# Kernel optimization log

Measured on AMD Instinct MI355X. Metric: run time of the kernel, lower is better.

Reference implementation:

```python
import jax, jax.numpy as jnp
import numpy as np

B, SQ, SK, D, H = 4, 2048, 2048, 1024, 16
HD = D // H


def setup_inputs() -> dict:
    key = jax.random.key(0)
    ks = jax.random.split(key, 8)
    s = 1.0 / np.sqrt(D)
    return {
        "query": jax.random.normal(ks[0], (B, SQ, D), jnp.float32),
        "key_value": jax.random.normal(ks[1], (B, SK, D), jnp.float32),
        "Wq": jax.random.normal(ks[2], (D, D), jnp.float32) * s,
        "bq": jnp.zeros((D,), jnp.float32),
        "Wkv": jax.random.normal(ks[3], (D, 2 * D), jnp.float32) * s,
        "bkv": jnp.zeros((2 * D,), jnp.float32),
        "Wo": jax.random.normal(ks[4], (D, D), jnp.float32) * s,
        "bo": jnp.zeros((D,), jnp.float32),
    }


def reference(query, key_value, Wq, bq, Wkv, bkv, Wo, bo):
    b, sq, _ = query.shape
    sk = key_value.shape[1]
    # Q projection -> [b, H, sq, HD]
    Q = (query @ Wq + bq).reshape(b, sq, H, HD).transpose(0, 2, 1, 3)
    # fused KV projection -> [b, sk, 2, H, HD]
    KV = (key_value @ Wkv + bkv).reshape(b, sk, 2, H, HD)
    K = KV[:, :, 0].transpose(0, 2, 1, 3)  # [b, H, sk, HD]
    V = KV[:, :, 1].transpose(0, 2, 1, 3)
    scale = 1.0 / np.sqrt(HD).astype(np.float32)
    scores = jnp.einsum("bhqd,bhkd->bhqk", Q, K) * scale
    attn = jax.nn.softmax(scores, axis=-1)  # dropout is identity in eval / p=0
    out = jnp.einsum("bhqk,bhkd->bhqd", attn, V)
    out = out.transpose(0, 2, 1, 3).reshape(b, sq, D)
    return out @ Wo + bo
```

## Files before the change

kernel.cpp:

```cpp
#include <hip/hip_runtime.h>
#include <hip/hip_bf16.h>
#include <stdint.h>


typedef __bf16 bf16_t;
typedef __bf16 bf16x8 __attribute__((ext_vector_type(8)));
typedef __bf16 bf16x4 __attribute__((ext_vector_type(4)));
typedef short  s16x4  __attribute__((ext_vector_type(4)));
typedef float  f32x4  __attribute__((ext_vector_type(4)));

#define MFMA16x32(a, b, c) __builtin_amdgcn_mfma_f32_16x16x32_bf16((a), (b), (c), 0, 0, 0)

__device__ __forceinline__ f32x4 mfma16x16(bf16x4 a, bf16x4 b, f32x4 c) {
#if __has_builtin(__builtin_amdgcn_mfma_f32_16x16x16_bf16)
    return __builtin_amdgcn_mfma_f32_16x16x16_bf16(a, b, c, 0, 0, 0);
#else
    return __builtin_amdgcn_mfma_f32_16x16x16bf16_1k(
        __builtin_bit_cast(s16x4, a), __builtin_bit_cast(s16x4, b), c, 0, 0, 0);
#endif
}

__device__ __forceinline__ float fast_exp2(float x) {
#if __has_builtin(__builtin_amdgcn_exp2f)
    return __builtin_amdgcn_exp2f(x);
#else
    return exp2f(x);
#endif
}

__device__ __forceinline__ void gload16(const void* g, const void* l) {
    __builtin_amdgcn_global_load_lds(
        (__attribute__((address_space(1))) void*)(uintptr_t)g,
        (__attribute__((address_space(3))) void*)(uintptr_t)l,
        16, 0, 0);
}

#define ATTN_SCALE 0.18033688011112042f

__global__ void cvt_bf16_2(const float* __restrict__ a, const float* __restrict__ b,
                           bf16_t* __restrict__ oa, bf16_t* __restrict__ ob) {
    int bid = blockIdx.x;
    const float* in;
    bf16_t* out;
    if (bid < 4096) { in = a; out = oa; }
    else            { in = b; out = ob; bid -= 4096; }
    int i = (bid * 256 + threadIdx.x) * 8;
    const float4* p = (const float4*)(in + i);
    float4 x = p[0], y = p[1];
    bf16x8 v;
    v[0] = (bf16_t)x.x; v[1] = (bf16_t)x.y; v[2] = (bf16_t)x.z; v[3] = (bf16_t)x.w;
    v[4] = (bf16_t)y.x; v[5] = (bf16_t)y.y; v[6] = (bf16_t)y.z; v[7] = (bf16_t)y.w;
    *(bf16x8*)(out + i) = v;
}

__global__ void transpose_cvt3(const float* __restrict__ Wq, const float* __restrict__ Wkv,
                               const float* __restrict__ Wo, bf16_t* __restrict__ WqT,
                               bf16_t* __restrict__ WkvT, bf16_t* __restrict__ WoT) {
    const float* W;
    bf16_t* WT;
    int N;
    if (blockIdx.z == 0)      { W = Wq;  WT = WqT;  N = 1024; }
    else if (blockIdx.z == 1) { W = Wkv; WT = WkvT; N = 2048; }
    else                      { W = Wo;  WT = WoT;  N = 1024; }
    if ((int)blockIdx.x * 64 >= N) return;
    const int K = 1024;
    __shared__ float tile[64][65];
    const int t = threadIdx.x;
    const int n0 = blockIdx.x * 64, k0 = blockIdx.y * 64;
#pragma unroll
    for (int i = 0; i < 16; ++i) {
        int idx = i * 256 + t;
        int r = idx >> 6, c = idx & 63;
        tile[r][c] = W[(size_t)(k0 + r) * N + n0 + c];
    }
    __syncthreads();
#pragma unroll
    for (int i = 0; i < 16; ++i) {
        int idx = i * 256 + t;
        int r = idx >> 6, c = idx & 63;
        WT[(size_t)(n0 + r) * K + k0 + c] = (bf16_t)tile[c][r];
    }
}

template <int MODE>
__global__ __launch_bounds__(256, 3)
void gemm_bt(const bf16_t* __restrict__ A, const bf16_t* __restrict__ BT,
             const float* __restrict__ bias, void* __restrict__ out0,
             void* __restrict__ out1, int M, int N, int K) {
    constexpr int SMEM = (MODE == 1) ? (16384 + 4 * 64 * 72 * 2) : 16384;
    __shared__ __align__(16) char pool[SMEM];
    bf16_t* sA = (bf16_t*)pool;
    bf16_t* sB = (bf16_t*)(pool + 8192);

    const int tid  = threadIdx.x;
    const int lane = tid & 63, w = tid >> 6;
    const int wr = w >> 1, wc = w & 1;
    const int quad = lane >> 4, l15 = lane & 15;
    const int x3 = l15 & 3;
    const int row0 = blockIdx.y * 128, col0 = blockIdx.x * 128;

    f32x4 acc[4][4];
    const f32x4 fz = {0.f, 0.f, 0.f, 0.f};
#pragma unroll
    for (int m = 0; m < 4; ++m)
#pragma unroll
        for (int n = 0; n < 4; ++n) acc[m][n] = fz;

    for (int kt = 0; kt < K; kt += 32) {
#pragma unroll
        for (int i = 0; i < 2; ++i) {
            int c = i * 256 + tid;
            int r = c >> 2, cr = c & 3;
            int g = cr ^ (r & 3);
            gload16(A + (size_t)(row0 + r) * K + kt + g * 8,
                    (const char*)sA + i * 4096 + w * 1024);
            gload16(BT + (size_t)(col0 + r) * K + kt + g * 8,
                    (const char*)sB + i * 4096 + w * 1024);
        }
        __syncthreads();

        bf16x8 af[4], bfr[4];
#pragma unroll
        for (int m = 0; m < 4; ++m)
            af[m] = *(const bf16x8*)(sA + (wr * 64 + m * 16 + l15) * 32 + (quad ^ x3) * 8);
#pragma unroll
        for (int n = 0; n < 4; ++n)
            bfr[n] = *(const bf16x8*)(sB + (wc * 64 + n * 16 + l15) * 32 + (quad ^ x3) * 8);
#pragma unroll
        for (int m = 0; m < 4; ++m)
#pragma unroll
            for (int n = 0; n < 4; ++n)
                acc[m][n] = MFMA16x32(af[m], bfr[n], acc[m][n]);
        __syncthreads();
    }

    if constexpr (MODE == 1) {
        if (col0 >= 1024) {
            bf16_t* sT = (bf16_t*)(pool + 16384) + w * (64 * 72);
            const int j0  = col0 - 1024 + wc * 64;
            const int hh  = j0 >> 6;
            const int sk0 = row0 + wr * 64;
            const int bb  = sk0 >> 11;
            const int skl = sk0 & 2047;
#pragma unroll
            for (int n = 0; n < 4; ++n) {
                int hd = n * 16 + l15;
                float bv = bias[1024 + j0 + n * 16 + l15];
#pragma unroll
                for (int m = 0; m < 4; ++m) {
                    bf16x4 v4;
                    v4[0] = (bf16_t)(acc[m][n][0] + bv);
                    v4[1] = (bf16_t)(acc[m][n][1] + bv);
                    v4[2] = (bf16_t)(acc[m][n][2] + bv);
                    v4[3] = (bf16_t)(acc[m][n][3] + bv);
                    *(bf16x4*)(sT + hd * 72 + m * 16 + quad * 4) = v4;
                }
            }
            bf16_t* vdst = (bf16_t*)out1 +
                           (((size_t)(bb * 16 + hh) * 64) << 11) + skl;
#pragma unroll
            for (int it = 0; it < 8; ++it) {
                int hd = it * 8 + (lane >> 3);
                int sc = (lane & 7) * 8;
                bf16x8 v = *(const bf16x8*)(sT + hd * 72 + sc);
                *(bf16x8*)(vdst + ((size_t)hd << 11) + sc) = v;
            }
            return;
        }
    }

#pragma unroll
    for (int m = 0; m < 4; ++m) {
        int rg_base = row0 + wr * 64 + m * 16 + quad * 4;
#pragma unroll
        for (int n = 0; n < 4; ++n) {
            int cg = col0 + wc * 64 + n * 16 + l15;
            float bv = bias[cg];
#pragma unroll
            for (int r = 0; r < 4; ++r) {
                int rg = rg_base + r;
                float v = acc[m][n][r] + bv;
                if constexpr (MODE == 2) {
                    ((float*)out0)[(size_t)rg * N + cg] = v;
                } else if constexpr (MODE == 0) {
                    v *= ATTN_SCALE;
                    int bb = rg >> 11, sq = rg & 2047;
                    int hh = cg >> 6, hd = cg & 63;
                    ((bf16_t*)out0)[(((size_t)(bb * 16 + hh) * 2048 + sq) << 6) | hd] =
                        (bf16_t)v;
                } else {
                    int bb = rg >> 11, sk = rg & 2047;
                    int hh = cg >> 6, hd = cg & 63;
                    ((bf16_t*)out0)[(((size_t)(bb * 16 + hh) * 2048 + sk) << 6) | hd] =
                        (bf16_t)v;
                }
            }
        }
    }
}

__global__ __launch_bounds__(256, 3)
void attn_kernel(const bf16_t* __restrict__ Qp, const bf16_t* __restrict__ Kb,
                 const bf16_t* __restrict__ Vt, bf16_t* __restrict__ Ob) {
    __shared__ __align__(16) char pool[40960];
    bf16_t* sQ   = (bf16_t*)pool;
    float*  redO = (float*)pool;
    float*  redL = (float*)(pool + 32768);

    const int tid = threadIdx.x;
    const int lane = tid & 63, w = tid >> 6;
    const int quad = lane >> 4, l15 = lane & 15;
    const int x7 = l15 & 7;
    const int qt = blockIdx.x, h = blockIdx.y, b = blockIdx.z;
    const size_t bh = (size_t)b * 16 + h;

    const bf16_t* Qg = Qp + bh * (2048 * 64) + (size_t)qt * (64 * 64);
    const bf16_t* Kg = Kb + bh * (2048 * 64);
    const bf16_t* Vg = Vt + bh * (64 * 2048);

    const int srow = tid >> 3;
    const int sg   = (tid & 7) ^ (srow & 7);

#pragma unroll
    for (int hh = 0; hh < 2; ++hh) {
        int row = hh * 32 + srow;
        gload16(Qg + (size_t)row * 64 + sg * 8, pool + hh * 4096 + w * 1024);
        gload16(Kg + (size_t)row * 64 + sg * 8, pool + 8192 + hh * 4096 + w * 1024);
        gload16(Vg + (size_t)row * 2048 + sg * 8, pool + 24576 + hh * 4096 + w * 1024);
    }
    __syncthreads();

    bf16x8 qf[4][2];
#pragma unroll
    for (int qb = 0; qb < 4; ++qb)
#pragma unroll
        for (int hh = 0; hh < 2; ++hh)
            qf[qb][hh] = *(const bf16x8*)(sQ + (qb * 16 + l15) * 64 +
                                          ((hh * 4 + quad) ^ x7) * 8);

    const f32x4 fz = {0.f, 0.f, 0.f, 0.f};
    f32x4 o_[4][4];
#pragma unroll
    for (int qb = 0; qb < 4; ++qb)
#pragma unroll
        for (int nh = 0; nh < 4; ++nh) o_[qb][nh] = fz;
    float lsum[4] = {0.f, 0.f, 0.f, 0.f};

    for (int t = 0; t < 32; ++t) {
        if (t < 31) {
            const bf16_t* Kt = Kg + (size_t)(t + 1) * (64 * 64);
            char* kb_ = pool + 8192 + ((t + 1) & 1) * 8192;
            char* vb_ = pool + 24576 + ((t + 1) & 1) * 8192;
#pragma unroll
            for (int hh = 0; hh < 2; ++hh) {
                int row = hh * 32 + srow;
                gload16(Kt + (size_t)row * 64 + sg * 8, kb_ + hh * 4096 + w * 1024);
                gload16(Vg + (size_t)row * 2048 + (t + 1) * 64 + sg * 8,
                        vb_ + hh * 4096 + w * 1024);
            }
        }
        const bf16_t* k0 = (const bf16_t*)(pool + 8192 + (t & 1) * 8192);
        const bf16_t* v0 = (const bf16_t*)(pool + 24576 + (t & 1) * 8192);

        const bf16_t* krow = k0 + (w * 16 + l15) * 64;
        bf16x8 kf0 = *(const bf16x8*)(krow + (quad ^ x7) * 8);
        bf16x8 kf1 = *(const bf16x8*)(krow + ((quad + 4) ^ x7) * 8);

        f32x4 s[4];
#pragma unroll
        for (int qb = 0; qb < 4; ++qb) {
            s[qb] = MFMA16x32(kf0, qf[qb][0], fz);
            s[qb] = MFMA16x32(kf1, qf[qb][1], s[qb]);
        }

        bf16x4 pf[4];
#pragma unroll
        for (int qb = 0; qb < 4; ++qb) {
            float p0 = fast_exp2(s[qb][0]);
            float p1 = fast_exp2(s[qb][1]);
            float p2 = fast_exp2(s[qb][2]);
            float p3 = fast_exp2(s[qb][3]);
            lsum[qb] += (p0 + p1) + (p2 + p3);
            bf16x4 pv = {(bf16_t)p0, (bf16_t)p1, (bf16_t)p2, (bf16_t)p3};
            pf[qb] = pv;
        }

        const int vslot = (2 * w + (quad >> 1)) ^ x7;
        const int vsub  = (quad & 1) * 4;
#pragma unroll
        for (int nh = 0; nh < 4; ++nh) {
            bf16x4 vf = *(const bf16x4*)(v0 + (nh * 16 + l15) * 64 + vslot * 8 + vsub);
#pragma unroll
            for (int qb = 0; qb < 4; ++qb)
                o_[qb][nh] = mfma16x16(pf[qb], vf, o_[qb][nh]);
        }
        __syncthreads();
    }

#pragma unroll
    for (int qb = 0; qb < 4; ++qb) {
        lsum[qb] += __shfl_xor(lsum[qb], 16);
        lsum[qb] += __shfl_xor(lsum[qb], 32);
    }
    if (quad == 0) {
#pragma unroll
        for (int qb = 0; qb < 4; ++qb) redL[w * 64 + qb * 16 + l15] = lsum[qb];
    }

    const int cq = tid >> 2;
    const int chb = (tid & 3) * 8;
    const size_t orow = (size_t)b * 2048 + (size_t)qt * 64 + cq;

#pragma unroll
    for (int ph = 0; ph < 2; ++ph) {
        __syncthreads();
#pragma unroll
        for (int qb = 0; qb < 4; ++qb)
#pragma unroll
            for (int nj = 0; nj < 2; ++nj) {
                int nh = ph * 2 + nj;
#pragma unroll
                for (int r = 0; r < 4; ++r)
                    redO[w * 2048 + (qb * 16 + quad * 4 + r) * 32 + nj * 16 + l15] =
                        o_[qb][nh][r];
            }
        __syncthreads();

        float lt = redL[cq] + redL[64 + cq] + redL[128 + cq] + redL[192 + cq];
        float linv = 1.f / lt;
        float4 a0 = {0, 0, 0, 0}, a1 = {0, 0, 0, 0};
#pragma unroll
        for (int ww = 0; ww < 4; ++ww) {
            const float4* p = (const float4*)(redO + ww * 2048 + cq * 32 + chb);
            float4 x = p[0], y = p[1];
            a0.x += x.x; a0.y += x.y; a0.z += x.z; a0.w += x.w;
            a1.x += y.x; a1.y += y.y; a1.z += y.z; a1.w += y.w;
        }
        bf16x8 ov;
        ov[0] = (bf16_t)(a0.x * linv); ov[1] = (bf16_t)(a0.y * linv);
        ov[2] = (bf16_t)(a0.z * linv); ov[3] = (bf16_t)(a0.w * linv);
        ov[4] = (bf16_t)(a1.x * linv); ov[5] = (bf16_t)(a1.y * linv);
        ov[6] = (bf16_t)(a1.z * linv); ov[7] = (bf16_t)(a1.w * linv);
        *(bf16x8*)(Ob + orow * 1024 + h * 64 + ph * 32 + chb) = ov;
    }
}

extern "C" void kernel_launch(void* const* d_in, const int* in_sizes, int n_in,
                              void* d_out, int out_size, void* d_ws, size_t ws_size,
                              hipStream_t stream) {
    const float* query     = (const float*)d_in[0];
    const float* key_value = (const float*)d_in[1];
    const float* Wq  = (const float*)d_in[2];
    const float* bq  = (const float*)d_in[3];
    const float* Wkv = (const float*)d_in[4];
    const float* bkv = (const float*)d_in[5];
    const float* Wo  = (const float*)d_in[6];
    const float* bo  = (const float*)d_in[7];
    float* out = (float*)d_out;

    char* ws = (char*)d_ws;
    const size_t MB = 1024 * 1024;
    bf16_t* WqT  = (bf16_t*)(ws + 0 * MB);
    bf16_t* WkvT = (bf16_t*)(ws + 2 * MB);
    bf16_t* WoT  = (bf16_t*)(ws + 6 * MB);
    bf16_t* qb   = (bf16_t*)(ws + 8 * MB);
    bf16_t* kvb  = (bf16_t*)(ws + 24 * MB);
    bf16_t* Qp   = (bf16_t*)(ws + 40 * MB);
    bf16_t* Kb   = (bf16_t*)(ws + 56 * MB);
    bf16_t* Vt   = (bf16_t*)(ws + 72 * MB);
    bf16_t* Ob   = (bf16_t*)(ws + 88 * MB);

    cvt_bf16_2<<<8192, 256, 0, stream>>>(query, key_value, qb, kvb);
    transpose_cvt3<<<dim3(32, 16, 3), 256, 0, stream>>>(Wq, Wkv, Wo, WqT, WkvT, WoT);

    gemm_bt<0><<<dim3(8, 64), 256, 0, stream>>>(qb, WqT, bq, Qp, nullptr,
                                                8192, 1024, 1024);
    gemm_bt<1><<<dim3(16, 64), 256, 0, stream>>>(kvb, WkvT, bkv, Kb, Vt,
                                                 8192, 2048, 1024);
    attn_kernel<<<dim3(32, 16, 4), 256, 0, stream>>>(Qp, Kb, Vt, Ob);
    gemm_bt<2><<<dim3(8, 64), 256, 0, stream>>>(Ob, WoT, bo, out, nullptr,
                                                8192, 1024, 1024);
}
```

Before: 333.7 us.

## Merge prep and QKV launches, move softmax row sums to MFMA, trim attention LDS

The two preprocessing kernels become one launch, and the Q and KV projection GEMMs become one grid, so fewer kernels run and the tail of one can overlap the head of the next. In attention, the softmax denominator is now accumulated by an MFMA against a ones vector, replacing VALU adds and cross-lane shuffles. The V double buffer reuses the Q staging area, which lowers LDS use so the launch bound can rise to 4 blocks per CU. Risks: the row sums are now taken from bf16-rounded probabilities, the added MFMA work competes with the PV product, and the larger occupancy target could cause register spills.

```diff
diff --git a/kernel.cpp b/kernel.cpp
--- a/kernel.cpp
+++ b/kernel.cpp
@@ -37,36 +37,40 @@
 
 #define ATTN_SCALE 0.18033688011112042f
 
-__global__ void cvt_bf16_2(const float* __restrict__ a, const float* __restrict__ b,
-                           bf16_t* __restrict__ oa, bf16_t* __restrict__ ob) {
+__global__ void prep_kernel(const float* __restrict__ q, const float* __restrict__ kv,
+                            const float* __restrict__ Wq, const float* __restrict__ Wkv,
+                            const float* __restrict__ Wo, bf16_t* __restrict__ qb,
+                            bf16_t* __restrict__ kvb, bf16_t* __restrict__ WqT,
+                            bf16_t* __restrict__ WkvT, bf16_t* __restrict__ WoT) {
+    __shared__ float tile[64][65];
     int bid = blockIdx.x;
-    const float* in;
-    bf16_t* out;
-    if (bid < 4096) { in = a; out = oa; }
-    else            { in = b; out = ob; bid -= 4096; }
-    int i = (bid * 256 + threadIdx.x) * 8;
-    const float4* p = (const float4*)(in + i);
-    float4 x = p[0], y = p[1];
-    bf16x8 v;
-    v[0] = (bf16_t)x.x; v[1] = (bf16_t)x.y; v[2] = (bf16_t)x.z; v[3] = (bf16_t)x.w;
-    v[4] = (bf16_t)y.x; v[5] = (bf16_t)y.y; v[6] = (bf16_t)y.z; v[7] = (bf16_t)y.w;
-    *(bf16x8*)(out + i) = v;
-}
-
-__global__ void transpose_cvt3(const float* __restrict__ Wq, const float* __restrict__ Wkv,
-                               const float* __restrict__ Wo, bf16_t* __restrict__ WqT,
-                               bf16_t* __restrict__ WkvT, bf16_t* __restrict__ WoT) {
+    const int t = threadIdx.x;
+    if (bid < 8192) {
+        const float* in;
+        bf16_t* out;
+        if (bid < 4096) { in = q; out = qb; }
+        else            { in = kv; out = kvb; bid -= 4096; }
+        int i = (bid * 256 + t) * 8;
+        const float4* p = (const float4*)(in + i);
+        float4 x = p[0], y = p[1];
+        bf16x8 v;
+        v[0] = (bf16_t)x.x; v[1] = (bf16_t)x.y; v[2] = (bf16_t)x.z; v[3] = (bf16_t)x.w;
+        v[4] = (bf16_t)y.x; v[5] = (bf16_t)y.y; v[6] = (bf16_t)y.z; v[7] = (bf16_t)y.w;
+        *(bf16x8*)(out + i) = v;
+        return;
+    }
+    bid -= 8192;
+    int z = bid >> 9, rem = bid & 511;
+    int xb = rem & 31, yb = rem >> 5;
     const float* W;
     bf16_t* WT;
     int N;
-    if (blockIdx.z == 0)      { W = Wq;  WT = WqT;  N = 1024; }
-    else if (blockIdx.z == 1) { W = Wkv; WT = WkvT; N = 2048; }
-    else                      { W = Wo;  WT = WoT;  N = 1024; }
-    if ((int)blockIdx.x * 64 >= N) return;
+    if (z == 0)      { W = Wq;  WT = WqT;  N = 1024; }
+    else if (z == 1) { W = Wkv; WT = WkvT; N = 2048; }
+    else             { W = Wo;  WT = WoT;  N = 1024; }
+    if (xb * 64 >= N) return;
     const int K = 1024;
-    __shared__ float tile[64][65];
-    const int t = threadIdx.x;
-    const int n0 = blockIdx.x * 64, k0 = blockIdx.y * 64;
+    const int n0 = xb * 64, k0 = yb * 64;
 #pragma unroll
     for (int i = 0; i < 16; ++i) {
         int idx = i * 256 + t;
@@ -82,13 +86,13 @@
     }
 }
 
-template <int MODE>
 __global__ __launch_bounds__(256, 3)
-void gemm_bt(const bf16_t* __restrict__ A, const bf16_t* __restrict__ BT,
-             const float* __restrict__ bias, void* __restrict__ out0,
-             void* __restrict__ out1, int M, int N, int K) {
-    constexpr int SMEM = (MODE == 1) ? (16384 + 4 * 64 * 72 * 2) : 16384;
-    __shared__ __align__(16) char pool[SMEM];
+void gemm_qkv(const bf16_t* __restrict__ qb, const bf16_t* __restrict__ kvb,
+              const bf16_t* __restrict__ WqT, const bf16_t* __restrict__ WkvT,
+              const float* __restrict__ bq, const float* __restrict__ bkv,
+              bf16_t* __restrict__ Qp, bf16_t* __restrict__ Kb,
+              bf16_t* __restrict__ Vt) {
+    __shared__ __align__(16) char pool[16384 + 4 * 64 * 72 * 2];
     bf16_t* sA = (bf16_t*)pool;
     bf16_t* sB = (bf16_t*)(pool + 8192);
 
@@ -97,7 +101,13 @@
     const int wr = w >> 1, wc = w & 1;
     const int quad = lane >> 4, l15 = lane & 15;
     const int x3 = l15 & 3;
-    const int row0 = blockIdx.y * 128, col0 = blockIdx.x * 128;
+    const bool isQ = blockIdx.x < 8;
+    const bf16_t* A    = isQ ? qb : kvb;
+    const bf16_t* BT   = isQ ? WqT : WkvT;
+    const float*  bias = isQ ? bq : bkv;
+    const int row0 = blockIdx.y * 128;
+    const int col0 = (isQ ? blockIdx.x : (blockIdx.x - 8)) * 128;
+    const int K = 1024;
 
     f32x4 acc[4][4];
     const f32x4 fz = {0.f, 0.f, 0.f, 0.f};
@@ -134,39 +144,36 @@
         __syncthreads();
     }
 
-    if constexpr (MODE == 1) {
-        if (col0 >= 1024) {
-            bf16_t* sT = (bf16_t*)(pool + 16384) + w * (64 * 72);
-            const int j0  = col0 - 1024 + wc * 64;
-            const int hh  = j0 >> 6;
-            const int sk0 = row0 + wr * 64;
-            const int bb  = sk0 >> 11;
-            const int skl = sk0 & 2047;
-#pragma unroll
-            for (int n = 0; n < 4; ++n) {
-                int hd = n * 16 + l15;
-                float bv = bias[1024 + j0 + n * 16 + l15];
-#pragma unroll
-                for (int m = 0; m < 4; ++m) {
-                    bf16x4 v4;
-                    v4[0] = (bf16_t)(acc[m][n][0] + bv);
-                    v4[1] = (bf16_t)(acc[m][n][1] + bv);
-                    v4[2] = (bf16_t)(acc[m][n][2] + bv);
-                    v4[3] = (bf16_t)(acc[m][n][3] + bv);
-                    *(bf16x4*)(sT + hd * 72 + m * 16 + quad * 4) = v4;
-                }
+    if (!isQ && col0 >= 1024) {
+        bf16_t* sT = (bf16_t*)(pool + 16384) + w * (64 * 72);
+        const int j0  = col0 - 1024 + wc * 64;
+        const int hh  = j0 >> 6;
+        const int sk0 = row0 + wr * 64;
+        const int bb  = sk0 >> 11;
+        const int skl = sk0 & 2047;
+#pragma unroll
+        for (int n = 0; n < 4; ++n) {
+            int hd = n * 16 + l15;
+            float bv = bkv[1024 + j0 + n * 16 + l15];
+#pragma unroll
+            for (int m = 0; m < 4; ++m) {
+                bf16x4 v4;
+                v4[0] = (bf16_t)(acc[m][n][0] + bv);
+                v4[1] = (bf16_t)(acc[m][n][1] + bv);
+                v4[2] = (bf16_t)(acc[m][n][2] + bv);
+                v4[3] = (bf16_t)(acc[m][n][3] + bv);
+                *(bf16x4*)(sT + hd * 72 + m * 16 + quad * 4) = v4;
             }
-            bf16_t* vdst = (bf16_t*)out1 +
-                           (((size_t)(bb * 16 + hh) * 64) << 11) + skl;
-#pragma unroll
-            for (int it = 0; it < 8; ++it) {
-                int hd = it * 8 + (lane >> 3);
-                int sc = (lane & 7) * 8;
-                bf16x8 v = *(const bf16x8*)(sT + hd * 72 + sc);
-                *(bf16x8*)(vdst + ((size_t)hd << 11) + sc) = v;
-            }
-            return;
-        }
+        }
+        bf16_t* vdst = Vt + (((size_t)(bb * 16 + hh) * 64) << 11) + skl;
+#pragma unroll
+        for (int it = 0; it < 8; ++it) {
+            int hd = it * 8 + (lane >> 3);
+            int sc = (lane & 7) * 8;
+            bf16x8 v = *(const bf16x8*)(sT + hd * 72 + sc);
+            *(bf16x8*)(vdst + ((size_t)hd << 11) + sc) = v;
+        }
+        return;
     }
 
 #pragma unroll
@@ -180,29 +187,82 @@
             for (int r = 0; r < 4; ++r) {
                 int rg = rg_base + r;
                 float v = acc[m][n][r] + bv;
-                if constexpr (MODE == 2) {
-                    ((float*)out0)[(size_t)rg * N + cg] = v;
-                } else if constexpr (MODE == 0) {
-                    v *= ATTN_SCALE;
-                    int bb = rg >> 11, sq = rg & 2047;
-                    int hh = cg >> 6, hd = cg & 63;
-                    ((bf16_t*)out0)[(((size_t)(bb * 16 + hh) * 2048 + sq) << 6) | hd] =
-                        (bf16_t)v;
-                } else {
-                    int bb = rg >> 11, sk = rg & 2047;
-                    int hh = cg >> 6, hd = cg & 63;
-                    ((bf16_t*)out0)[(((size_t)(bb * 16 + hh) * 2048 + sk) << 6) | hd] =
-                        (bf16_t)v;
-                }
+                int bb = rg >> 11, sr = rg & 2047;
+                int hh = cg >> 6, hd = cg & 63;
+                size_t idx = (((size_t)(bb * 16 + hh) * 2048 + sr) << 6) | hd;
+                if (isQ) Qp[idx] = (bf16_t)(v * ATTN_SCALE);
+                else     Kb[idx] = (bf16_t)v;
             }
         }
     }
 }
 
 __global__ __launch_bounds__(256, 3)
+void gemm_out(const bf16_t* __restrict__ A, const bf16_t* __restrict__ BT,
+              const float* __restrict__ bias, float* __restrict__ out,
+              int M, int N, int K) {
+    __shared__ __align__(16) bf16_t sA[128 * 32];
+    __shared__ __align__(16) bf16_t sB[128 * 32];
+    const int tid  = threadIdx.x;
+    const int lane = tid & 63, w = tid >> 6;
+    const int wr = w >> 1, wc = w & 1;
+    const int quad = lane >> 4, l15 = lane & 15;
+    const int x3 = l15 & 3;
+    const int row0 = blockIdx.y * 128, col0 = blockIdx.x * 128;
+
+    f32x4 acc[4][4];
+    const f32x4 fz = {0.f, 0.f, 0.f, 0.f};
+#pragma unroll
+    for (int m = 0; m < 4; ++m)
+#pragma unroll
+        for (int n = 0; n < 4; ++n) acc[m][n] = fz;
+
+    for (int kt = 0; kt < K; kt += 32) {
+#pragma unroll
+        for (int i = 0; i < 2; ++i) {
+            int c = i * 256 + tid;
+            int r = c >> 2, cr = c & 3;
+            int g = cr ^ (r & 3);
+            gload16(A + (size_t)(row0 + r) * K + kt + g * 8,
+                    (const char*)sA + i * 4096 + w * 1024);
+            gload16(BT + (size_t)(col0 + r) * K + kt + g * 8,
+                    (const char*)sB + i * 4096 + w * 1024);
+        }
+        __syncthreads();
+
+        bf16x8 af[4], bfr[4];
+#pragma unroll
+        for (int m = 0; m < 4; ++m)
+            af[m] = *(const bf16x8*)(sA + (wr * 64 + m * 16 + l15) * 32 + (quad ^ x3) * 8);
+#pragma unroll
+        for (int n = 0; n < 4; ++n)
+            bfr[n] = *(const bf16x8*)(sB + (wc * 64 + n * 16 + l15) * 32 + (quad ^ x3) * 8);
+#pragma unroll
+        for (int m = 0; m < 4; ++m)
+#pragma unroll
+            for (int n = 0; n < 4; ++n)
+                acc[m][n] = MFMA16x32(af[m], bfr[n], acc[m][n]);
+        __syncthreads();
+    }
+
+#pragma unroll
+    for (int m = 0; m < 4; ++m) {
+        int rg_base = row0 + wr * 64 + m * 16 + quad * 4;
+#pragma unroll
+        for (int n = 0; n < 4; ++n) {
+            int cg = col0 + wc * 64 + n * 16 + l15;
+            float bv = bias[cg];
+#pragma unroll
+            for (int r = 0; r < 4; ++r)
+                out[(size_t)(rg_base + r) * N + cg] = acc[m][n][r] + bv;
+        }
+    }
+}
+
+__global__ __launch_bounds__(256, 4)
 void attn_kernel(const bf16_t* __restrict__ Qp, const bf16_t* __restrict__ Kb,
                  const bf16_t* __restrict__ Vt, bf16_t* __restrict__ Ob) {
-    __shared__ __align__(16) char pool[40960];
+    __shared__ __align__(16) char pool[36864];
     bf16_t* sQ   = (bf16_t*)pool;
     float*  redO = (float*)pool;
     float*  redL = (float*)(pool + 32768);
@@ -237,20 +297,24 @@
         for (int hh = 0; hh < 2; ++hh)
             qf[qb][hh] = *(const bf16x8*)(sQ + (qb * 16 + l15) * 64 +
                                           ((hh * 4 + quad) ^ x7) * 8);
+    __syncthreads();
 
     const f32x4 fz = {0.f, 0.f, 0.f, 0.f};
+    const bf16x4 ones = {(bf16_t)1.f, (bf16_t)1.f, (bf16_t)1.f, (bf16_t)1.f};
     f32x4 o_[4][4];
-#pragma unroll
-    for (int qb = 0; qb < 4; ++qb)
+    f32x4 lacc[4];
+#pragma unroll
+    for (int qb = 0; qb < 4; ++qb) {
+        lacc[qb] = fz;
 #pragma unroll
         for (int nh = 0; nh < 4; ++nh) o_[qb][nh] = fz;
-    float lsum[4] = {0.f, 0.f, 0.f, 0.f};
+    }
 
     for (int t = 0; t < 32; ++t) {
         if (t < 31) {
             const bf16_t* Kt = Kg + (size_t)(t + 1) * (64 * 64);
-            char* kb_ = pool + 8192 + ((t + 1) & 1) * 8192;
-            char* vb_ = pool + 24576 + ((t + 1) & 1) * 8192;
+            char* kb_ = pool + 8192 + (((t + 1) & 1) << 13);
+            char* vb_ = ((t + 1) & 1) ? pool : pool + 24576;
 #pragma unroll
             for (int hh = 0; hh < 2; ++hh) {
                 int row = hh * 32 + srow;
@@ -259,8 +323,8 @@
                         vb_ + hh * 4096 + w * 1024);
             }
         }
-        const bf16_t* k0 = (const bf16_t*)(pool + 8192 + (t & 1) * 8192);
-        const bf16_t* v0 = (const bf16_t*)(pool + 24576 + (t & 1) * 8192);
+        const bf16_t* k0 = (const bf16_t*)(pool + 8192 + ((t & 1) << 13));
+        const bf16_t* v0 = (const bf16_t*)((t & 1) ? pool : pool + 24576);
 
         const bf16_t* krow = k0 + (w * 16 + l15) * 64;
         bf16x8 kf0 = *(const bf16x8*)(krow + (quad ^ x7) * 8);
@@ -276,13 +340,13 @@
         bf16x4 pf[4];
 #pragma unroll
         for (int qb = 0; qb < 4; ++qb) {
-            float p0 = fast_exp2(s[qb][0]);
-            float p1 = fast_exp2(s[qb][1]);
-            float p2 = fast_exp2(s[qb][2]);
-            float p3 = fast_exp2(s[qb][3]);
-            lsum[qb] += (p0 + p1) + (p2 + p3);
-            bf16x4 pv = {(bf16_t)p0, (bf16_t)p1, (bf16_t)p2, (bf16_t)p3};
+            bf16x4 pv;
+            pv[0] = (bf16_t)fast_exp2(s[qb][0]);
+            pv[1] = (bf16_t)fast_exp2(s[qb][1]);
+            pv[2] = (bf16_t)fast_exp2(s[qb][2]);
+            pv[3] = (bf16_t)fast_exp2(s[qb][3]);
             pf[qb] = pv;
+            lacc[qb] = mfma16x16(pf[qb], ones, lacc[qb]);
         }
 
         const int vslot = (2 * w + (quad >> 1)) ^ x7;
@@ -297,14 +361,12 @@
         __syncthreads();
     }
 
-#pragma unroll
-    for (int qb = 0; qb < 4; ++qb) {
-        lsum[qb] += __shfl_xor(lsum[qb], 16);
-        lsum[qb] += __shfl_xor(lsum[qb], 32);
-    }
-    if (quad == 0) {
-#pragma unroll
-        for (int qb = 0; qb < 4; ++qb) redL[w * 64 + qb * 16 + l15] = lsum[qb];
+    if (l15 == 0) {
+#pragma unroll
+        for (int qb = 0; qb < 4; ++qb)
+#pragma unroll
+            for (int r = 0; r < 4; ++r)
+                redL[w * 64 + qb * 16 + quad * 4 + r] = lacc[qb][r];
     }
 
     const int cq = tid >> 2;
@@ -370,14 +432,10 @@
     bf16_t* Vt   = (bf16_t*)(ws + 72 * MB);
     bf16_t* Ob   = (bf16_t*)(ws + 88 * MB);
 
-    cvt_bf16_2<<<8192, 256, 0, stream>>>(query, key_value, qb, kvb);
-    transpose_cvt3<<<dim3(32, 16, 3), 256, 0, stream>>>(Wq, Wkv, Wo, WqT, WkvT, WoT);
-
-    gemm_bt<0><<<dim3(8, 64), 256, 0, stream>>>(qb, WqT, bq, Qp, nullptr,
-                                                8192, 1024, 1024);
-    gemm_bt<1><<<dim3(16, 64), 256, 0, stream>>>(kvb, WkvT, bkv, Kb, Vt,
-                                                 8192, 2048, 1024);
+    prep_kernel<<<9728, 256, 0, stream>>>(query, key_value, Wq, Wkv, Wo,
+                                          qb, kvb, WqT, WkvT, WoT);
+    gemm_qkv<<<dim3(24, 64), 256, 0, stream>>>(qb, kvb, WqT, WkvT, bq, bkv,
+                                               Qp, Kb, Vt);
     attn_kernel<<<dim3(32, 16, 4), 256, 0, stream>>>(Qp, Kb, Vt, Ob);
-    gemm_bt<2><<<dim3(8, 64), 256, 0, stream>>>(Ob, WoT, bo, out, nullptr,
-                                                8192, 1024, 1024);
-}
+    gemm_out<<<dim3(8, 64), 256, 0, stream>>>(Ob, WoT, bo, out, 8192, 1024, 1024);
+}
```

Result: slower. 481.9 us (+44.4%).
